# Optimization experiments

Measured on AMD Instinct MI355X. Metric: run time of the kernel, lower is better.

## Reference

```python
import jax, jax.numpy as jnp
import numpy as np

B, H, W, DM = 32, 32, 32, 128   # batch, height, width, d_model
DIN, N, R = 64, 16, 8           # d_inner(low_dim), d_state, dt_rank=ceil(128/16)
LN_EPS = 1e-5


def setup_inputs() -> dict:
    key = jax.random.key(0)
    ks = jax.random.split(key, 10)
    x = jax.random.normal(ks[0], (B, H, W, DM), dtype=jnp.float32)
    w_in = jax.random.normal(ks[1], (2 * DIN, DM), dtype=jnp.float32) * 0.02
    conv_w = jax.random.normal(ks[2], (DIN, 1, 3, 3), dtype=jnp.float32) * 0.1
    conv_b = jax.random.normal(ks[3], (DIN,), dtype=jnp.float32) * 0.01
    xproj_w = jax.random.normal(ks[4], (R + 2 * N, DIN), dtype=jnp.float32) * 0.05
    dtproj_w = jax.random.uniform(ks[5], (DIN, R), dtype=jnp.float32,
                                  minval=-(R ** -0.5), maxval=R ** -0.5)
    # dt bias init: inverse-softplus of dt ~ LogUniform(1e-3, 0.1)
    dt = jnp.exp(jax.random.uniform(ks[6], (DIN,)) * (np.log(0.1) - np.log(0.001)) + np.log(0.001))
    dt = jnp.clip(dt, 1e-4, None)
    dtproj_b = dt + jnp.log(-jnp.expm1(-dt))
    A_logs = jnp.log(jnp.broadcast_to(jnp.arange(1, N + 1, dtype=jnp.float32), (DIN, N)))
    Ds = jnp.ones((DIN,), dtype=jnp.float32)
    ln_g = jnp.ones((DIN,), dtype=jnp.float32)
    ln_b = jnp.zeros((DIN,), dtype=jnp.float32)
    w_out = jax.random.normal(ks[7], (DM, DIN), dtype=jnp.float32) * 0.02
    return {"x": x, "w_in": w_in, "conv_w": conv_w, "conv_b": conv_b,
            "xproj_w": xproj_w, "dtproj_w": dtproj_w, "dtproj_b": dtproj_b,
            "A_logs": A_logs, "Ds": Ds, "ln_g": ln_g, "ln_b": ln_b, "w_out": w_out}


def _silu(v):
    return v * jax.nn.sigmoid(v)


def reference(x, w_in, conv_w, conv_b, xproj_w, dtproj_w, dtproj_b,
              A_logs, Ds, ln_g, ln_b, w_out):
    b, h, w, _ = x.shape
    L = h * w
    # in_proj (no bias) and gate split
    xz = jnp.einsum('bhwc,ec->bhwe', x, w_in)           # [B,H,W,2*DIN]
    xc, z = jnp.split(xz, 2, axis=-1)
    # depthwise conv2d, SAME padding (k=3, pad=1), then SiLU
    xc = jnp.transpose(xc, (0, 3, 1, 2))                # [B,DIN,H,W]
    xc = jax.lax.conv_general_dilated(
        xc, conv_w, window_strides=(1, 1), padding=((1, 1), (1, 1)),
        feature_group_count=DIN, dimension_numbers=('NCHW', 'OIHW', 'NCHW'))
    xc = _silu(xc + conv_b[None, :, None, None])
    u = xc.reshape(b, DIN, L)                            # [B,D,L]
    # x_proj -> dt, B, C
    x_dbl = jnp.einsum('bdl,cd->bcl', u, xproj_w)        # [B,R+2N,L]
    dts, Bs, Cs = x_dbl[:, :R], x_dbl[:, R:R + N], x_dbl[:, R + N:]
    delta = jnp.einsum('brl,dr->bdl', dts, dtproj_w) + dtproj_b[None, :, None]
    delta = jax.nn.softplus(delta)                       # [B,D,L]
    A = -jnp.exp(A_logs)                                 # [D,N]
    dA = jnp.exp(delta[..., None] * A[None, :, None, :])               # [B,D,L,N]
    dBu = (delta * u)[..., None] * jnp.swapaxes(Bs, 1, 2)[:, None]     # [B,D,L,N]
    # sequential selective scan over L
    dA_s = jnp.moveaxis(dA, 2, 0)                        # [L,B,D,N]
    dBu_s = jnp.moveaxis(dBu, 2, 0)
    C_s = jnp.moveaxis(Cs, 2, 0)                         # [L,B,N]

    def step(hst, inp):
        dA_t, dBu_t, C_t = inp
        hst = dA_t * hst + dBu_t                         # [B,D,N]
        y_t = jnp.einsum('bdn,bn->bd', hst, C_t)
        return hst, y_t

    h0 = jnp.zeros((b, DIN, N), dtype=u.dtype)
    _, ys = jax.lax.scan(step, h0, (dA_s, dBu_s, C_s))   # ys: [L,B,D]
    y = jnp.moveaxis(ys, 0, 2) + Ds[None, :, None] * u   # [B,D,L]
    # back to [B,H,W,D], layernorm, gate, out_proj
    y = jnp.swapaxes(y, 1, 2).reshape(b, h, w, DIN)
    mu = jnp.mean(y, axis=-1, keepdims=True)
    var = jnp.var(y, axis=-1, keepdims=True)
    y = (y - mu) * jax.lax.rsqrt(var + LN_EPS) * ln_g + ln_b
    y = y * _silu(z)
    return jnp.einsum('bhwd,cd->bhwc', y, w_out)
```

## Files before the change

kernel.cpp:

```cpp
#include <hip/hip_runtime.h>


__global__ __launch_bounds__(256) void k1_gemm_in(
    const float* __restrict__ x, const float* __restrict__ w_in,
    float* __restrict__ xc, float* __restrict__ z)
{
    __shared__ float As[32 * 68];
    __shared__ float Ws[32 * 132];
    const int t  = threadIdx.x;
    const int p0 = blockIdx.x * 64;
    const int tx = t & 15, ty = t >> 4;

    float acc[4][8];
#pragma unroll
    for (int i = 0; i < 4; ++i)
#pragma unroll
        for (int j = 0; j < 8; ++j) acc[i][j] = 0.f;

    for (int kk = 0; kk < 128; kk += 32) {
        {
            const int m  = t >> 3;
            const int c4 = (t & 7) * 4;
            const float4 v0 = *reinterpret_cast<const float4*>(&x[(size_t)(p0 + m) * 128 + kk + c4]);
            const float4 v1 = *reinterpret_cast<const float4*>(&x[(size_t)(p0 + m + 32) * 128 + kk + c4]);
            As[(c4 + 0) * 68 + m] = v0.x; As[(c4 + 1) * 68 + m] = v0.y;
            As[(c4 + 2) * 68 + m] = v0.z; As[(c4 + 3) * 68 + m] = v0.w;
            As[(c4 + 0) * 68 + m + 32] = v1.x; As[(c4 + 1) * 68 + m + 32] = v1.y;
            As[(c4 + 2) * 68 + m + 32] = v1.z; As[(c4 + 3) * 68 + m + 32] = v1.w;
        }
        for (int i = t; i < 4096; i += 256) {
            const int c = i & 31, e = i >> 5;
            Ws[c * 132 + e] = w_in[(size_t)e * 128 + kk + c];
        }
        __syncthreads();
#pragma unroll
        for (int k = 0; k < 32; ++k) {
            const float4 a  = *reinterpret_cast<const float4*>(&As[k * 68 + (ty << 2)]);
            const float4 b0 = *reinterpret_cast<const float4*>(&Ws[k * 132 + (tx << 3)]);
            const float4 b1 = *reinterpret_cast<const float4*>(&Ws[k * 132 + (tx << 3) + 4]);
            const float am[4] = {a.x, a.y, a.z, a.w};
            const float bm[8] = {b0.x, b0.y, b0.z, b0.w, b1.x, b1.y, b1.z, b1.w};
#pragma unroll
            for (int i = 0; i < 4; ++i)
#pragma unroll
                for (int j = 0; j < 8; ++j)
                    acc[i][j] = fmaf(am[i], bm[j], acc[i][j]);
        }
        __syncthreads();
    }

    const int b  = p0 >> 10;
    const int l0 = (p0 & 1023) + (ty << 2);
    if (tx < 8) {
#pragma unroll
        for (int j = 0; j < 8; ++j) {
            const int e = (tx << 3) + j;
            *reinterpret_cast<float4*>(&xc[((size_t)b * 64 + e) * 1024 + l0]) =
                make_float4(acc[0][j], acc[1][j], acc[2][j], acc[3][j]);
        }
    } else {
        const int d0 = (tx - 8) << 3;
#pragma unroll
        for (int i = 0; i < 4; ++i) {
            const size_t p = (size_t)p0 + (ty << 2) + i;
            *reinterpret_cast<float4*>(&z[p * 64 + d0]) =
                make_float4(acc[i][0], acc[i][1], acc[i][2], acc[i][3]);
            *reinterpret_cast<float4*>(&z[p * 64 + d0 + 4]) =
                make_float4(acc[i][4], acc[i][5], acc[i][6], acc[i][7]);
        }
    }
}

__global__ __launch_bounds__(256) void k2_conv(
    const float* __restrict__ xc, const float* __restrict__ cw,
    const float* __restrict__ cb, float* __restrict__ u)
{
    __shared__ float pl[1024];
    const int bd = blockIdx.x;
    const int t  = threadIdx.x;
    const int d  = bd & 63;
    reinterpret_cast<float4*>(pl)[t] =
        reinterpret_cast<const float4*>(xc + (size_t)bd * 1024)[t];
    float w[9];
#pragma unroll
    for (int i = 0; i < 9; ++i) w[i] = cw[d * 9 + i];
    const float bias = cb[d];
    __syncthreads();
    float o[4];
#pragma unroll
    for (int i = 0; i < 4; ++i) {
        const int p  = t * 4 + i;
        const int py = p >> 5, px = p & 31;
        float s = 0.f;
#pragma unroll
        for (int ky = 0; ky < 3; ++ky) {
            const int iy = py + ky - 1;
            if (iy < 0 || iy > 31) continue;
#pragma unroll
            for (int kx = 0; kx < 3; ++kx) {
                const int ix = px + kx - 1;
                if (ix < 0 || ix > 31) continue;
                s = fmaf(pl[iy * 32 + ix], w[ky * 3 + kx], s);
            }
        }
        s += bias;
        o[i] = s / (1.f + __expf(-s));
    }
    reinterpret_cast<float4*>(u + (size_t)bd * 1024)[t] = make_float4(o[0], o[1], o[2], o[3]);
}

__global__ __launch_bounds__(64) void k3_xproj(
    const float* __restrict__ u, const float* __restrict__ xpw,
    const float* __restrict__ dtw_g, const float* __restrict__ dtb,
    float* __restrict__ delta, float* __restrict__ Bsp, float* __restrict__ Csp)
{
    __shared__ float ut[64][36];
    __shared__ float xw[64 * 40];
    __shared__ float xd8[8][36];
    __shared__ float dwv[64 * 9];
    const int t   = threadIdx.x;
    const int blk = blockIdx.x;
    const int b   = blk >> 5;
    const int l0  = (blk & 31) * 32;

#pragma unroll 4
    for (int c = 0; c < 40; ++c)
        xw[t * 40 + c] = xpw[(size_t)c * 64 + t];
#pragma unroll
    for (int k = 0; k < 8; ++k)
        dwv[t * 9 + k] = dtw_g[t * 8 + k];
    {
        const float* ub = u + (size_t)b * 65536 + l0;
#pragma unroll
        for (int i = t; i < 512; i += 64) {
            const int dd = i >> 3, pq = i & 7;
            const float4 v = *reinterpret_cast<const float4*>(ub + (size_t)dd * 1024 + pq * 4);
            *reinterpret_cast<float4*>(&ut[dd][pq * 4]) = v;
        }
    }
    __syncthreads();

    const int pixq = t & 7;
    const int cg   = t >> 3;
    const int c0   = cg * 5;
    float4 acc[5];
#pragma unroll
    for (int j = 0; j < 5; ++j) acc[j] = make_float4(0.f, 0.f, 0.f, 0.f);
#pragma unroll 8
    for (int dd = 0; dd < 64; ++dd) {
        const float4 uv = *reinterpret_cast<const float4*>(&ut[dd][pixq * 4]);
        const float* row = &xw[dd * 40 + c0];
#pragma unroll
        for (int j = 0; j < 5; ++j) {
            const float w = row[j];
            acc[j].x = fmaf(w, uv.x, acc[j].x);
            acc[j].y = fmaf(w, uv.y, acc[j].y);
            acc[j].z = fmaf(w, uv.z, acc[j].z);
            acc[j].w = fmaf(w, uv.w, acc[j].w);
        }
    }
#pragma unroll
    for (int j = 0; j < 5; ++j) {
        const int c = c0 + j;
        if (c < 8) {
            *reinterpret_cast<float4*>(&xd8[c][pixq * 4]) = acc[j];
        } else if (c < 24) {
            *reinterpret_cast<float4*>(Bsp + (size_t)b * 16384 +
                (size_t)(c - 8) * 1024 + l0 + pixq * 4) = acc[j];
        } else {
            *reinterpret_cast<float4*>(Csp + (size_t)b * 16384 +
                (size_t)(c - 24) * 1024 + l0 + pixq * 4) = acc[j];
        }
    }
    __syncthreads();

    const int dg = t >> 3;
    float dts[4][8];
#pragma unroll
    for (int e = 0; e < 4; ++e)
#pragma unroll
        for (int r = 0; r < 8; ++r)
            dts[e][r] = xd8[r][pixq * 4 + e];
    float* dp = delta + (size_t)b * 65536 + l0 + pixq * 4;
#pragma unroll
    for (int k = 0; k < 8; ++k) {
        const int dd = dg * 8 + k;
        const float* r8 = &dwv[dd * 9];
        const float bias = dtb[dd];
        float ov[4];
#pragma unroll
        for (int e = 0; e < 4; ++e) {
            float s = bias;
#pragma unroll
            for (int r = 0; r < 8; ++r) s = fmaf(dts[e][r], r8[r], s);
            ov[e] = fmaxf(s, 0.f) + log1pf(__expf(-fabsf(s)));
        }
        *reinterpret_cast<float4*>(dp + (size_t)dd * 1024) =
            make_float4(ov[0], ov[1], ov[2], ov[3]);
    }
}

__global__ __launch_bounds__(256) void k4_scan(
    const float* __restrict__ delta, const float* __restrict__ u,
    const float* __restrict__ Bsp, const float* __restrict__ Csp,
    const float* __restrict__ A_logs, const float* __restrict__ Ds,
    float* __restrict__ y)
{
    __shared__ float Ps[256][17];
    __shared__ float qs[256][17];
    __shared__ float Sp[16][17];
    __shared__ float Sq[16][17];
    const int t = threadIdx.x;
    const int pair = blockIdx.x;
    const int b = pair >> 6, d = pair & 63;

    float A[16];
#pragma unroll
    for (int n = 0; n < 16; ++n) A[n] = -__expf(A_logs[d * 16 + n]);

    const float4 d4 = *reinterpret_cast<const float4*>(delta + (size_t)pair * 1024 + t * 4);
    const float4 u4 = *reinterpret_cast<const float4*>(u     + (size_t)pair * 1024 + t * 4);
    const float du0 = d4.x * u4.x, du1 = d4.y * u4.y;
    const float du2 = d4.z * u4.z, du3 = d4.w * u4.w;

    const float* Bb = Bsp + (size_t)b * 16384 + t * 4;
    const float* Cb = Csp + (size_t)b * 16384 + t * 4;

#pragma unroll
    for (int n = 0; n < 16; ++n) {
        const float4 B4 = *reinterpret_cast<const float4*>(Bb + n * 1024);
        float a, P, q;
        a = __expf(d4.x * A[n]); P = a;   q = du0 * B4.x;
        a = __expf(d4.y * A[n]); P *= a;  q = fmaf(a, q, du1 * B4.y);
        a = __expf(d4.z * A[n]); P *= a;  q = fmaf(a, q, du2 * B4.z);
        a = __expf(d4.w * A[n]); P *= a;  q = fmaf(a, q, du3 * B4.w);
        Ps[t][n] = P; qs[t][n] = q;
    }
    __syncthreads();

    const int n = t >> 4, g = t & 15;
    float rp[16], rq[16];
    {
        float Pseg = 1.f, qseg = 0.f;
#pragma unroll
        for (int i = 0; i < 16; ++i) {
            const int c = g * 16 + i;
            rp[i] = Ps[c][n]; rq[i] = qs[c][n];
            qseg = fmaf(rp[i], qseg, rq[i]);
            Pseg *= rp[i];
        }
        Sp[g][n] = Pseg; Sq[g][n] = qseg;
    }
    __syncthreads();
    if (t < 16) {
        float h = 0.f;
#pragma unroll
        for (int s = 0; s < 16; ++s) {
            const float Pv = Sp[s][t], qv = Sq[s][t];
            Sp[s][t] = h;
            h = fmaf(Pv, h, qv);
        }
    }
    __syncthreads();
    {
        float h = Sp[g][n];
#pragma unroll
        for (int i = 0; i < 16; ++i) {
            const int c = g * 16 + i;
            qs[c][n] = h;
            h = fmaf(rp[i], h, rq[i]);
        }
    }
    __syncthreads();

    const float Dval = Ds[d];
    float y0 = Dval * u4.x, y1 = Dval * u4.y, y2 = Dval * u4.z, y3 = Dval * u4.w;
#pragma unroll
    for (int nn = 0; nn < 16; ++nn) {
        const float4 B4 = *reinterpret_cast<const float4*>(Bb + nn * 1024);
        const float4 C4 = *reinterpret_cast<const float4*>(Cb + nn * 1024);
        float h = qs[t][nn];
        float a;
        a = __expf(d4.x * A[nn]); h = fmaf(a, h, du0 * B4.x); y0 = fmaf(h, C4.x, y0);
        a = __expf(d4.y * A[nn]); h = fmaf(a, h, du1 * B4.y); y1 = fmaf(h, C4.y, y1);
        a = __expf(d4.z * A[nn]); h = fmaf(a, h, du2 * B4.z); y2 = fmaf(h, C4.z, y2);
        a = __expf(d4.w * A[nn]); h = fmaf(a, h, du3 * B4.w); y3 = fmaf(h, C4.w, y3);
    }
    *reinterpret_cast<float4*>(y + (size_t)pair * 1024 + t * 4) =
        make_float4(y0, y1, y2, y3);
}

__global__ __launch_bounds__(256) void k5_out(
    const float* __restrict__ y, const float* __restrict__ z,
    const float* __restrict__ ln_g, const float* __restrict__ ln_b,
    const float* __restrict__ w_out, float* __restrict__ out)
{
    __shared__ float yn[64 * 68];
    __shared__ float wo[64 * 132];
    const int t  = threadIdx.x;
    const int p0 = blockIdx.x * 64;
    const int b  = p0 >> 10, l0 = p0 & 1023;

    for (int i = t; i < 8192; i += 256) {
        const int c = i >> 6, dd = i & 63;
        wo[dd * 132 + c] = w_out[i];
    }

    {
        const int d = t >> 2;
        const float* yrow = y + ((size_t)b * 64 + d) * 1024 + l0;
#pragma unroll
        for (int k = 0; k < 4; ++k) {
            const int c4 = ((t & 3) + k * 4) * 4;
            const float4 v = *reinterpret_cast<const float4*>(&yrow[c4]);
            yn[(c4 + 0) * 68 + d] = v.x;
            yn[(c4 + 1) * 68 + d] = v.y;
            yn[(c4 + 2) * 68 + d] = v.z;
            yn[(c4 + 3) * 68 + d] = v.w;
        }
    }
    __syncthreads();

    const int lane = t & 63, wv = t >> 6;
    const float g = ln_g[lane], bbv = ln_b[lane];
#pragma unroll 1
    for (int i = 0; i < 16; ++i) {
        const int pl = wv * 16 + i;
        const size_t p = (size_t)p0 + pl;
        const float v  = yn[pl * 68 + lane];
        const float zv = z[p * 64 + lane];
        float s1 = v, s2 = v * v;
#pragma unroll
        for (int m = 1; m < 64; m <<= 1) {
            s1 += __shfl_xor(s1, m);
            s2 += __shfl_xor(s2, m);
        }
        const float mu   = s1 * (1.f / 64.f);
        const float var  = s2 * (1.f / 64.f) - mu * mu;
        const float rstd = rsqrtf(var + 1e-5f);
        const float sz   = zv / (1.f + __expf(-zv));
        yn[pl * 68 + lane] = ((v - mu) * rstd * g + bbv) * sz;
    }
    __syncthreads();

    const int tx = t & 31, ty = t >> 5;
    float acc[8][4];
#pragma unroll
    for (int i = 0; i < 8; ++i)
#pragma unroll
        for (int j = 0; j < 4; ++j) acc[i][j] = 0.f;

    for (int dd = 0; dd < 64; ++dd) {
        const float4 w4 = *reinterpret_cast<const float4*>(&wo[dd * 132 + (tx << 2)]);
#pragma unroll
        for (int i = 0; i < 8; ++i) {
            const float a = yn[(ty * 8 + i) * 68 + dd];
            acc[i][0] = fmaf(a, w4.x, acc[i][0]);
            acc[i][1] = fmaf(a, w4.y, acc[i][1]);
            acc[i][2] = fmaf(a, w4.z, acc[i][2]);
            acc[i][3] = fmaf(a, w4.w, acc[i][3]);
        }
    }
#pragma unroll
    for (int i = 0; i < 8; ++i) {
        const size_t p = (size_t)p0 + ty * 8 + i;
        *reinterpret_cast<float4*>(&out[p * 128 + (tx << 2)]) =
            make_float4(acc[i][0], acc[i][1], acc[i][2], acc[i][3]);
    }
}

extern "C" void kernel_launch(void* const* d_in, const int* in_sizes, int n_in,
                              void* d_out, int out_size, void* d_ws, size_t ws_size,
                              hipStream_t stream)
{
    const float* x        = (const float*)d_in[0];
    const float* w_in     = (const float*)d_in[1];
    const float* conv_w   = (const float*)d_in[2];
    const float* conv_b   = (const float*)d_in[3];
    const float* xproj_w  = (const float*)d_in[4];
    const float* dtproj_w = (const float*)d_in[5];
    const float* dtproj_b = (const float*)d_in[6];
    const float* A_logs   = (const float*)d_in[7];
    const float* Ds       = (const float*)d_in[8];
    const float* ln_g     = (const float*)d_in[9];
    const float* ln_b     = (const float*)d_in[10];
    const float* w_out    = (const float*)d_in[11];
    float* out = (float*)d_out;
    float* ws  = (float*)d_ws;

    const size_t M  = (size_t)2097152;
    float* xc    = ws;
    float* z     = ws + M;
    float* u     = ws + 2 * M;
    float* delta = ws + 3 * M;
    float* y     = ws + 4 * M;
    float* Bsp   = ws + 5 * M;
    float* Csp   = Bsp + 524288;

    k1_gemm_in<<<512, 256, 0, stream>>>(x, w_in, xc, z);
    k2_conv<<<2048, 256, 0, stream>>>(xc, conv_w, conv_b, u);
    k3_xproj<<<1024, 64, 0, stream>>>(u, xproj_w, dtproj_w, dtproj_b, delta, Bsp, Csp);
    k4_scan<<<2048, 256, 0, stream>>>(delta, u, Bsp, Csp, A_logs, Ds, y);
    k5_out<<<512, 256, 0, stream>>>(y, z, ln_g, ln_b, w_out, out);
}
```

Measured before the change: 101.8 us.

## Use bf16x3 split MFMA for input projection GEMM

Replaces the FP32 SIMT register-tiled GEMM in the input projection with MFMA 16x16x32 bf16 instructions. It keeps near-FP32 accuracy by splitting each operand into hi/lo bf16 parts and accumulating three products. Operands are loaded straight from global memory into registers rather than staged through shared memory. Results go through an LDS tile so the transposed xc and the z outputs can be written coalesced. This trades some precision (dropping the lo*lo term) and redundant weight loads per wave for matrix-core throughput on one of several kernels.

```diff
diff --git a/kernel.cpp b/kernel.cpp
--- a/kernel.cpp
+++ b/kernel.cpp
@@ -1,73 +1,89 @@
 #include <hip/hip_runtime.h>
 
+
+typedef __attribute__((ext_vector_type(8))) short short8;
+typedef __attribute__((ext_vector_type(4))) float floatx4;
+
+__device__ __forceinline__ void cvt_split8(const float* v, short8& hi, short8& lo) {
+#pragma unroll
+    for (int i = 0; i < 8; ++i) {
+        const unsigned xb = __float_as_uint(v[i]);
+        hi[i] = (short)(xb >> 16);
+        const float lf = v[i] - __uint_as_float(xb & 0xFFFF0000u);
+        lo[i] = (short)(__float_as_uint(lf) >> 16);
+    }
+}
 
 __global__ __launch_bounds__(256) void k1_gemm_in(
     const float* __restrict__ x, const float* __restrict__ w_in,
     float* __restrict__ xc, float* __restrict__ z)
 {
-    __shared__ float As[32 * 68];
-    __shared__ float Ws[32 * 132];
-    const int t  = threadIdx.x;
-    const int p0 = blockIdx.x * 64;
-    const int tx = t & 15, ty = t >> 4;
-
-    float acc[4][8];
-#pragma unroll
-    for (int i = 0; i < 4; ++i)
-#pragma unroll
-        for (int j = 0; j < 8; ++j) acc[i][j] = 0.f;
-
-    for (int kk = 0; kk < 128; kk += 32) {
+    __shared__ float Cls[64 * 132];
+    const int t    = threadIdx.x;
+    const int p0   = blockIdx.x * 64;
+    const int w    = t >> 6;
+    const int l    = t & 63;
+    const int lrow = l & 15, lk = l >> 4;
+    const int m0   = w * 16;
+
+    floatx4 acc[8];
+#pragma unroll
+    for (int nt = 0; nt < 8; ++nt) acc[nt] = (floatx4){0.f, 0.f, 0.f, 0.f};
+
+#pragma unroll
+    for (int ks = 0; ks < 4; ++ks) {
+        const int k0 = ks * 32 + lk * 8;
+        float av[8];
         {
-            const int m  = t >> 3;
-            const int c4 = (t & 7) * 4;
-            const float4 v0 = *reinterpret_cast<const float4*>(&x[(size_t)(p0 + m) * 128 + kk + c4]);
-            const float4 v1 = *reinterpret_cast<const float4*>(&x[(size_t)(p0 + m + 32) * 128 + kk + c4]);
-            As[(c4 + 0) * 68 + m] = v0.x; As[(c4 + 1) * 68 + m] = v0.y;
-            As[(c4 + 2) * 68 + m] = v0.z; As[(c4 + 3) * 68 + m] = v0.w;
-            As[(c4 + 0) * 68 + m + 32] = v1.x; As[(c4 + 1) * 68 + m + 32] = v1.y;
-            As[(c4 + 2) * 68 + m + 32] = v1.z; As[(c4 + 3) * 68 + m + 32] = v1.w;
-        }
-        for (int i = t; i < 4096; i += 256) {
-            const int c = i & 31, e = i >> 5;
-            Ws[c * 132 + e] = w_in[(size_t)e * 128 + kk + c];
-        }
-        __syncthreads();
-#pragma unroll
-        for (int k = 0; k < 32; ++k) {
-            const float4 a  = *reinterpret_cast<const float4*>(&As[k * 68 + (ty << 2)]);
-            const float4 b0 = *reinterpret_cast<const float4*>(&Ws[k * 132 + (tx << 3)]);
-            const float4 b1 = *reinterpret_cast<const float4*>(&Ws[k * 132 + (tx << 3) + 4]);
-            const float am[4] = {a.x, a.y, a.z, a.w};
-            const float bm[8] = {b0.x, b0.y, b0.z, b0.w, b1.x, b1.y, b1.z, b1.w};
-#pragma unroll
-            for (int i = 0; i < 4; ++i)
-#pragma unroll
-                for (int j = 0; j < 8; ++j)
-                    acc[i][j] = fmaf(am[i], bm[j], acc[i][j]);
-        }
-        __syncthreads();
-    }
-
-    const int b  = p0 >> 10;
-    const int l0 = (p0 & 1023) + (ty << 2);
-    if (tx < 8) {
-#pragma unroll
-        for (int j = 0; j < 8; ++j) {
-            const int e = (tx << 3) + j;
-            *reinterpret_cast<float4*>(&xc[((size_t)b * 64 + e) * 1024 + l0]) =
-                make_float4(acc[0][j], acc[1][j], acc[2][j], acc[3][j]);
-        }
-    } else {
-        const int d0 = (tx - 8) << 3;
-#pragma unroll
-        for (int i = 0; i < 4; ++i) {
-            const size_t p = (size_t)p0 + (ty << 2) + i;
-            *reinterpret_cast<float4*>(&z[p * 64 + d0]) =
-                make_float4(acc[i][0], acc[i][1], acc[i][2], acc[i][3]);
-            *reinterpret_cast<float4*>(&z[p * 64 + d0 + 4]) =
-                make_float4(acc[i][4], acc[i][5], acc[i][6], acc[i][7]);
-        }
+            const float* ap = x + (size_t)(p0 + m0 + lrow) * 128 + k0;
+            *reinterpret_cast<float4*>(&av[0]) = *reinterpret_cast<const float4*>(ap);
+            *reinterpret_cast<float4*>(&av[4]) = *reinterpret_cast<const float4*>(ap + 4);
+        }
+        short8 ahi, alo;
+        cvt_split8(av, ahi, alo);
+#pragma unroll
+        for (int nt = 0; nt < 8; ++nt) {
+            float bv[8];
+            const float* bp = w_in + (size_t)(nt * 16 + lrow) * 128 + k0;
+            *reinterpret_cast<float4*>(&bv[0]) = *reinterpret_cast<const float4*>(bp);
+            *reinterpret_cast<float4*>(&bv[4]) = *reinterpret_cast<const float4*>(bp + 4);
+            short8 bhi, blo;
+            cvt_split8(bv, bhi, blo);
+            acc[nt] = __builtin_amdgcn_mfma_f32_16x16x32_bf16(ahi, bhi, acc[nt], 0, 0, 0);
+            acc[nt] = __builtin_amdgcn_mfma_f32_16x16x32_bf16(ahi, blo, acc[nt], 0, 0, 0);
+            acc[nt] = __builtin_amdgcn_mfma_f32_16x16x32_bf16(alo, bhi, acc[nt], 0, 0, 0);
+        }
+    }
+
+#pragma unroll
+    for (int nt = 0; nt < 8; ++nt)
+#pragma unroll
+        for (int r = 0; r < 4; ++r)
+            Cls[(m0 + lk * 4 + r) * 132 + nt * 16 + lrow] = acc[nt][r];
+    __syncthreads();
+
+    const int b = p0 >> 10, lbase = p0 & 1023;
+    {
+        const int e  = t >> 2;
+        const int pg = (t & 3) * 16;
+        float tmp[16];
+#pragma unroll
+        for (int j = 0; j < 16; ++j) tmp[j] = Cls[(pg + j) * 132 + e];
+        float* dst = xc + ((size_t)b * 64 + e) * 1024 + lbase + pg;
+#pragma unroll
+        for (int q = 0; q < 4; ++q)
+            *reinterpret_cast<float4*>(dst + q * 4) =
+                make_float4(tmp[q*4], tmp[q*4+1], tmp[q*4+2], tmp[q*4+3]);
+    }
+    {
+        const int pix = t >> 2;
+        const int dq  = (t & 3) * 16;
+        const float* srcr = &Cls[pix * 132 + 64 + dq];
+        float* dst = z + ((size_t)p0 + pix) * 64 + dq;
+#pragma unroll
+        for (int q = 0; q < 4; ++q)
+            *reinterpret_cast<float4*>(dst + q * 4) =
+                *reinterpret_cast<const float4*>(srcr + q * 4);
     }
 }
 
```

Result: no change. 103.7 us (+1.9%).

## Fuse depthwise conv+SiLU with x_proj/dt_proj into one kernel per row-pair tile

Applied to the files above, without the earlier changes.

Merges the depthwise 3x3 conv kernel and the x_proj/dt_proj kernel into one kernel. Each block loads a two-row tile plus halo rows of xc for all 64 channels into shared memory, computes u, and feeds it straight into the projection. This removes one launch and the re-read of u from global memory. The cost is a larger shared-memory footprint, fewer blocks (512), and redundant halo loads and weight staging per block.

```diff
diff --git a/kernel.cpp b/kernel.cpp
--- a/kernel.cpp
+++ b/kernel.cpp
@@ -71,132 +71,124 @@
     }
 }
 
-__global__ __launch_bounds__(256) void k2_conv(
+__global__ __launch_bounds__(256) void k23_conv_xproj(
     const float* __restrict__ xc, const float* __restrict__ cw,
-    const float* __restrict__ cb, float* __restrict__ u)
-{
-    __shared__ float pl[1024];
-    const int bd = blockIdx.x;
-    const int t  = threadIdx.x;
-    const int d  = bd & 63;
-    reinterpret_cast<float4*>(pl)[t] =
-        reinterpret_cast<const float4*>(xc + (size_t)bd * 1024)[t];
-    float w[9];
-#pragma unroll
-    for (int i = 0; i < 9; ++i) w[i] = cw[d * 9 + i];
-    const float bias = cb[d];
-    __syncthreads();
-    float o[4];
-#pragma unroll
-    for (int i = 0; i < 4; ++i) {
-        const int p  = t * 4 + i;
-        const int py = p >> 5, px = p & 31;
-        float s = 0.f;
-#pragma unroll
-        for (int ky = 0; ky < 3; ++ky) {
-            const int iy = py + ky - 1;
-            if (iy < 0 || iy > 31) continue;
-#pragma unroll
-            for (int kx = 0; kx < 3; ++kx) {
-                const int ix = px + kx - 1;
-                if (ix < 0 || ix > 31) continue;
-                s = fmaf(pl[iy * 32 + ix], w[ky * 3 + kx], s);
-            }
-        }
-        s += bias;
-        o[i] = s / (1.f + __expf(-s));
-    }
-    reinterpret_cast<float4*>(u + (size_t)bd * 1024)[t] = make_float4(o[0], o[1], o[2], o[3]);
-}
-
-__global__ __launch_bounds__(64) void k3_xproj(
-    const float* __restrict__ u, const float* __restrict__ xpw,
+    const float* __restrict__ cb, const float* __restrict__ xpw,
     const float* __restrict__ dtw_g, const float* __restrict__ dtb,
-    float* __restrict__ delta, float* __restrict__ Bsp, float* __restrict__ Csp)
-{
-    __shared__ float ut[64][36];
+    float* __restrict__ u, float* __restrict__ delta,
+    float* __restrict__ Bsp, float* __restrict__ Csp)
+{
+    __shared__ float xct[64][132];
+    __shared__ float ut[64][68];
     __shared__ float xw[64 * 40];
-    __shared__ float xd8[8][36];
+    __shared__ float xd8[8][68];
+    __shared__ float wls[64][10];
+    __shared__ float cbl[64];
     __shared__ float dwv[64 * 9];
+
     const int t   = threadIdx.x;
     const int blk = blockIdx.x;
-    const int b   = blk >> 5;
-    const int l0  = (blk & 31) * 32;
-
-#pragma unroll 4
-    for (int c = 0; c < 40; ++c)
-        xw[t * 40 + c] = xpw[(size_t)c * 64 + t];
-#pragma unroll
-    for (int k = 0; k < 8; ++k)
-        dwv[t * 9 + k] = dtw_g[t * 8 + k];
-    {
-        const float* ub = u + (size_t)b * 65536 + l0;
-#pragma unroll
-        for (int i = t; i < 512; i += 64) {
-            const int dd = i >> 3, pq = i & 7;
-            const float4 v = *reinterpret_cast<const float4*>(ub + (size_t)dd * 1024 + pq * 4);
-            *reinterpret_cast<float4*>(&ut[dd][pq * 4]) = v;
-        }
-    }
-    __syncthreads();
-
-    const int pixq = t & 7;
-    const int cg   = t >> 3;
-    const int c0   = cg * 5;
-    float4 acc[5];
-#pragma unroll
-    for (int j = 0; j < 5; ++j) acc[j] = make_float4(0.f, 0.f, 0.f, 0.f);
+    const int b   = blk >> 4;
+    const int s   = blk & 15;
+    const int l0  = s * 64;
+
+    for (int i = t; i < 576; i += 256) wls[i / 9][i % 9] = cw[i];
+    if (t < 64) cbl[t] = cb[t];
+    for (int i = t; i < 2560; i += 256) {
+        const int dd = i / 40, c = i - dd * 40;
+        xw[dd * 40 + c] = xpw[(size_t)c * 64 + dd];
+    }
+    for (int i = t; i < 512; i += 256) dwv[(i >> 3) * 9 + (i & 7)] = dtw_g[i];
+
+    {
+        const int d = t >> 2, q = t & 3;
+        const float* src = xc + ((size_t)b * 64 + d) * 1024 + (2 * s - 1) * 32;
+        float* dst = &xct[d][0];
+#pragma unroll
+        for (int k = 0; k < 8; ++k) {
+            const int j  = k * 4 + q;
+            const int rr = 2 * s - 1 + (j >> 3);
+            float4 v = make_float4(0.f, 0.f, 0.f, 0.f);
+            if (rr >= 0 && rr < 32)
+                v = *reinterpret_cast<const float4*>(src + j * 4);
+            *reinterpret_cast<float4*>(dst + j * 4) = v;
+        }
+    }
+    __syncthreads();
+
+    {
+        const int p  = t & 63;
+        const int py = p >> 5, px = p & 31;
+        const int dg = t >> 6;
+#pragma unroll
+        for (int kd = 0; kd < 16; ++kd) {
+            const int d = dg * 16 + kd;
+            float sacc = cbl[d];
+#pragma unroll
+            for (int ky = 0; ky < 3; ++ky) {
+#pragma unroll
+                for (int kx = 0; kx < 3; ++kx) {
+                    const int xx = px + kx - 1;
+                    if (xx >= 0 && xx < 32)
+                        sacc = fmaf(xct[d][(py + ky) * 32 + xx],
+                                    wls[d][ky * 3 + kx], sacc);
+                }
+            }
+            const float uv = sacc / (1.f + __expf(-sacc));
+            ut[d][p] = uv;
+            u[((size_t)b * 64 + d) * 1024 + l0 + p] = uv;
+        }
+    }
+    __syncthreads();
+
+    {
+        const int p2 = (t & 31) * 2;
+        const int c0 = (t >> 5) * 5;
+        float2 acc[5];
+#pragma unroll
+        for (int j = 0; j < 5; ++j) acc[j] = make_float2(0.f, 0.f);
 #pragma unroll 8
-    for (int dd = 0; dd < 64; ++dd) {
-        const float4 uv = *reinterpret_cast<const float4*>(&ut[dd][pixq * 4]);
-        const float* row = &xw[dd * 40 + c0];
+        for (int dd = 0; dd < 64; ++dd) {
+            const float2 uv = *reinterpret_cast<const float2*>(&ut[dd][p2]);
+            const float* row = &xw[dd * 40 + c0];
+#pragma unroll
+            for (int j = 0; j < 5; ++j) {
+                acc[j].x = fmaf(row[j], uv.x, acc[j].x);
+                acc[j].y = fmaf(row[j], uv.y, acc[j].y);
+            }
+        }
 #pragma unroll
         for (int j = 0; j < 5; ++j) {
-            const float w = row[j];
-            acc[j].x = fmaf(w, uv.x, acc[j].x);
-            acc[j].y = fmaf(w, uv.y, acc[j].y);
-            acc[j].z = fmaf(w, uv.z, acc[j].z);
-            acc[j].w = fmaf(w, uv.w, acc[j].w);
-        }
-    }
-#pragma unroll
-    for (int j = 0; j < 5; ++j) {
-        const int c = c0 + j;
-        if (c < 8) {
-            *reinterpret_cast<float4*>(&xd8[c][pixq * 4]) = acc[j];
-        } else if (c < 24) {
-            *reinterpret_cast<float4*>(Bsp + (size_t)b * 16384 +
-                (size_t)(c - 8) * 1024 + l0 + pixq * 4) = acc[j];
-        } else {
-            *reinterpret_cast<float4*>(Csp + (size_t)b * 16384 +
-                (size_t)(c - 24) * 1024 + l0 + pixq * 4) = acc[j];
-        }
-    }
-    __syncthreads();
-
-    const int dg = t >> 3;
-    float dts[4][8];
-#pragma unroll
-    for (int e = 0; e < 4; ++e)
-#pragma unroll
-        for (int r = 0; r < 8; ++r)
-            dts[e][r] = xd8[r][pixq * 4 + e];
-    float* dp = delta + (size_t)b * 65536 + l0 + pixq * 4;
-#pragma unroll
-    for (int k = 0; k < 8; ++k) {
-        const int dd = dg * 8 + k;
-        const float* r8 = &dwv[dd * 9];
-        const float bias = dtb[dd];
-        float ov[4];
-#pragma unroll
-        for (int e = 0; e < 4; ++e) {
-            float s = bias;
-#pragma unroll
-            for (int r = 0; r < 8; ++r) s = fmaf(dts[e][r], r8[r], s);
-            ov[e] = fmaxf(s, 0.f) + log1pf(__expf(-fabsf(s)));
-        }
-        *reinterpret_cast<float4*>(dp + (size_t)dd * 1024) =
-            make_float4(ov[0], ov[1], ov[2], ov[3]);
+            const int c = c0 + j;
+            if (c < 8) {
+                *reinterpret_cast<float2*>(&xd8[c][p2]) = acc[j];
+            } else if (c < 24) {
+                *reinterpret_cast<float2*>(Bsp + (size_t)b * 16384 +
+                    (size_t)(c - 8) * 1024 + l0 + p2) = acc[j];
+            } else {
+                *reinterpret_cast<float2*>(Csp + (size_t)b * 16384 +
+                    (size_t)(c - 24) * 1024 + l0 + p2) = acc[j];
+            }
+        }
+    }
+    __syncthreads();
+
+    {
+        const int p  = t & 63;
+        const int dg = t >> 6;
+        float dts[8];
+#pragma unroll
+        for (int r = 0; r < 8; ++r) dts[r] = xd8[r][p];
+        float* dp = delta + (size_t)b * 65536 + l0 + p;
+#pragma unroll
+        for (int kd = 0; kd < 16; ++kd) {
+            const int dd = dg * 16 + kd;
+            const float* r8 = &dwv[dd * 9];
+            float sv = dtb[dd];
+#pragma unroll
+            for (int r = 0; r < 8; ++r) sv = fmaf(dts[r], r8[r], sv);
+            dp[(size_t)dd * 1024] = fmaxf(sv, 0.f) + log1pf(__expf(-fabsf(sv)));
+        }
     }
 }
 
@@ -398,8 +390,8 @@
     float* Csp   = Bsp + 524288;
 
     k1_gemm_in<<<512, 256, 0, stream>>>(x, w_in, xc, z);
-    k2_conv<<<2048, 256, 0, stream>>>(xc, conv_w, conv_b, u);
-    k3_xproj<<<1024, 64, 0, stream>>>(u, xproj_w, dtproj_w, dtproj_b, delta, Bsp, Csp);
+    k23_conv_xproj<<<512, 256, 0, stream>>>(xc, conv_w, conv_b, xproj_w,
+                                            dtproj_w, dtproj_b, u, delta, Bsp, Csp);
     k4_scan<<<2048, 256, 0, stream>>>(delta, u, Bsp, Csp, A_logs, Ds, y);
     k5_out<<<512, 256, 0, stream>>>(y, z, ln_g, ln_b, w_out, out);
 }
```

New measurement: 100.6 us. No clear change (-1.1%).
